# Performance work log

Measured on AMD Instinct MI355X. Metric: run time of the kernel, lower is better.

## Reference

```python
import jax, jax.numpy as jnp
import numpy as np

V = 50000   # nodes
E = 600000  # edges
D = 256     # node_feat_size == graph_feat_size
K = 20      # hardcoded Kronecker projection dim
OUT = 256   # out_dim

def layer_norm(x, g, b, eps=1e-5):
    mu = jnp.mean(x, axis=-1, keepdims=True)
    var = jnp.var(x, axis=-1, keepdims=True)
    return (x - mu) * jax.lax.rsqrt(var + eps) * g + b

def setup_inputs() -> dict:
    key = jax.random.key(0)
    ks = jax.random.split(key, 12)
    def rn(k, shape, s=0.05):
        return jax.random.normal(k, shape, dtype=jnp.float32) * s
    return dict(
        node_feats=jax.random.normal(ks[0], (V, D), dtype=jnp.float32),
        src=jax.random.randint(ks[1], (E,), 0, V),
        dst=jax.random.randint(ks[2], (E,), 0, V),
        # KroneckerMessage.proj_node: Linear(D,20)+LN(20)
        Wp=rn(ks[3], (D, K)), bp=jnp.zeros((K,), jnp.float32),
        gp=jnp.ones((K,), jnp.float32), betap=jnp.zeros((K,), jnp.float32),
        # KroneckerMessage.proj_kron: Linear(400,OUT)+LN(OUT)
        Wk=rn(ks[4], (K * K, OUT)), bk=jnp.zeros((OUT,), jnp.float32),
        gk=jnp.ones((OUT,), jnp.float32), betak=jnp.zeros((OUT,), jnp.float32),
        # project_edge: Linear(2D,1)
        We=rn(ks[5], (2 * D, 1)), be=jnp.zeros((1,), jnp.float32),
        # AttentiveGRU2.project_node: Linear(D, graph_feat_size=D)
        Wn=rn(ks[6], (D, D)), bn=jnp.zeros((D,), jnp.float32),
        # GRUCell(input=D, hidden=D), torch layout [3H, in]
        W_ih=rn(ks[7], (3 * D, D)), W_hh=rn(ks[8], (3 * D, D)),
        b_ih=jnp.zeros((3 * D,), jnp.float32), b_hh=jnp.zeros((3 * D,), jnp.float32),
        # layer_norm after GRU
        g_ln=jnp.ones((D,), jnp.float32), beta_ln=jnp.zeros((D,), jnp.float32),
        # concat_proj: Linear(D+OUT, D)+LN(D)
        Wc=rn(ks[9], (D + OUT, D)), bc=jnp.zeros((D,), jnp.float32),
        gc=jnp.ones((D,), jnp.float32), betac=jnp.zeros((D,), jnp.float32),
    )

def reference(node_feats, src, dst, Wp, bp, gp, betap, Wk, bk, gk, betak,
              We, be, Wn, bn, W_ih, W_hh, b_ih, b_hh, g_ln, beta_ln,
              Wc, bc, gc, betac):
    Vn = node_feats.shape[0]
    En = src.shape[0]
    # --- KroneckerMessage branch ---
    npj = jax.nn.relu(layer_norm(node_feats @ Wp + bp, gp, betap))        # [V, 20]
    kron = jnp.einsum('ea,ek->eak', npj[src], npj[dst]).reshape(En, -1)    # [E, 400]
    kron = jax.nn.relu(layer_norm(kron @ Wk + bk, gk, betak))              # [E, OUT]
    kron_feat = jax.ops.segment_sum(kron, dst, num_segments=Vn)           # [V, OUT]
    # --- edge attention logits (he = [dst_hv, src_hv]) ---
    he = jnp.concatenate([node_feats[dst], node_feats[src]], axis=1)       # [E, 2D]
    logits = jax.nn.relu(he @ We + be)                                     # [E, 1]
    # --- edge softmax grouped by destination node ---
    m = jax.ops.segment_max(logits, dst, num_segments=Vn)                  # [V, 1]
    ex = jnp.exp(logits - m[dst])
    denom = jax.ops.segment_sum(ex, dst, num_segments=Vn)
    a = ex / denom[dst]                                                    # [E, 1]
    # --- weighted src-feature aggregation ---
    hv = node_feats @ Wn + bn                                              # [V, D]
    context = jax.nn.relu(jax.ops.segment_sum(hv[src] * a, dst, num_segments=Vn))
    # --- GRUCell(context, node_feats), torch semantics ---
    gi = context @ W_ih.T + b_ih
    gh = node_feats @ W_hh.T + b_hh
    i_r, i_z, i_n = jnp.split(gi, 3, axis=1)
    h_r, h_z, h_n = jnp.split(gh, 3, axis=1)
    r = jax.nn.sigmoid(i_r + h_r)
    z = jax.nn.sigmoid(i_z + h_z)
    n = jnp.tanh(i_n + r * h_n)
    h = (1.0 - z) * n + z * node_feats
    gru_out = layer_norm(jax.nn.relu(h), g_ln, beta_ln)                    # [V, D]
    # --- concat + projection ---
    cat = jnp.concatenate([gru_out, kron_feat], axis=1)                    # [V, D+OUT]
    return jax.nn.relu(layer_norm(cat @ Wc + bc, gc, betac))               # [V, D]
```

## Files before the change

### kernel.cpp

```cpp
#include <hip/hip_runtime.h>
#include <hip/hip_bf16.h>
#include <math.h>

#define KG 8
#define KTHR 512
#define KCHUNK 128

typedef __attribute__((ext_vector_type(8))) short bfrag;
typedef __attribute__((ext_vector_type(4))) float cfrag;
typedef _Float16 __attribute__((ext_vector_type(2))) half2v;

__device__ __forceinline__ ushort f2bf(float f) {
    __hip_bfloat16 h = __float2bfloat16(f);
    return *(ushort*)&h;
}
__device__ __forceinline__ float bf2f(ushort u) {
    __hip_bfloat16 h;
    *(ushort*)&h = u;
    return __bfloat162float(h);
}
__device__ __forceinline__ uint packf16(float lo, float hi) {
    _Float16 l = (_Float16)lo, h = (_Float16)hi;
    ushort ul = *(ushort*)&l, uh = *(ushort*)&h;
    return (uint)ul | ((uint)uh << 16);
}

__device__ __forceinline__ void blockSum2(float& s1, float& s2, float* red) {
    #pragma unroll
    for (int off = 32; off > 0; off >>= 1) {
        s1 += __shfl_xor(s1, off);
        s2 += __shfl_xor(s2, off);
    }
    int lane = threadIdx.x & 63, wid = threadIdx.x >> 6;
    if (lane == 0) { red[wid] = s1; red[4 + wid] = s2; }
    __syncthreads();
    s1 = red[0] + red[1] + red[2] + red[3];
    s2 = red[4] + red[5] + red[6] + red[7];
}

__device__ __forceinline__ float dppWaveSum(float x) {
    float t;
    t = __int_as_float(__builtin_amdgcn_update_dpp(0, __float_as_int(x), 0x111, 0xf, 0xf, true)); x += t;
    t = __int_as_float(__builtin_amdgcn_update_dpp(0, __float_as_int(x), 0x112, 0xf, 0xf, true)); x += t;
    t = __int_as_float(__builtin_amdgcn_update_dpp(0, __float_as_int(x), 0x114, 0xf, 0xf, true)); x += t;
    t = __int_as_float(__builtin_amdgcn_update_dpp(0, __float_as_int(x), 0x118, 0xf, 0xf, true)); x += t;
    t = __int_as_float(__builtin_amdgcn_update_dpp(0, __float_as_int(x), 0x142, 0xf, 0xf, true)); x += t;
    t = __int_as_float(__builtin_amdgcn_update_dpp(0, __float_as_int(x), 0x143, 0xf, 0xf, true)); x += t;
    return __int_as_float(__builtin_amdgcn_readlane(__float_as_int(x), 63));
}

__device__ __forceinline__ float sigmoidf(float x) { return 1.0f / (1.0f + expf(-x)); }

__global__ __launch_bounds__(256) void cast_bf16_kernel(
    const float* __restrict__ x, ushort* __restrict__ y, int n)
{
    int i = (blockIdx.x * 256 + threadIdx.x) * 4;
    if (i < n) {
        float4 v = *(const float4*)(x + i);
        ushort4 o;
        o.x = f2bf(v.x); o.y = f2bf(v.y); o.z = f2bf(v.z); o.w = f2bf(v.w);
        *(ushort4*)(y + i) = o;
    }
}

__global__ __launch_bounds__(256) void prep_w_kernel(
    const float* __restrict__ Wn, const float* __restrict__ Wih,
    const float* __restrict__ Whh, const float* __restrict__ Wc,
    const float* __restrict__ b_ih, const float* __restrict__ b_hh,
    const float* __restrict__ Wp, const float* __restrict__ bp,
    const float* __restrict__ Wk,
    ushort* __restrict__ BTn, ushort* __restrict__ BTrz,
    ushort* __restrict__ BTin, ushort* __restrict__ BThn,
    ushort* __restrict__ BTc, float* __restrict__ bias_rz,
    ushort* __restrict__ BTp, float* __restrict__ bp_pad,
    uint* __restrict__ Wkp)
{
    int id = blockIdx.x * 256 + threadIdx.x;
    if (id < 262144) {
        int n = id >> 9, k = id & 511;
        float v = (k < 256) ? Wih[n * 256 + k] : Whh[n * 256 + k - 256];
        BTrz[id] = f2bf(v);
    } else if (id < 327680) {
        int j = id - 262144; int n = j >> 8, k = j & 255;
        BTin[j] = f2bf(Wih[(512 + n) * 256 + k]);
    } else if (id < 393216) {
        int j = id - 327680; int n = j >> 8, k = j & 255;
        BThn[j] = f2bf(Whh[(512 + n) * 256 + k]);
    } else if (id < 458752) {
        int j = id - 393216; int n = j >> 8, k = j & 255;
        BTn[j] = f2bf(Wn[k * 256 + n]);
    } else if (id < 589824) {
        int j = id - 458752; int n = j >> 9, k = j & 511;
        BTc[j] = f2bf(Wc[k * 256 + n]);
    } else if (id < 590336) {
        int n = id - 589824;
        bias_rz[n] = b_ih[n] + b_hh[n];
    } else if (id < 623104) {
        int j = id - 590336; int n = j >> 8, k = j & 255;
        BTp[j] = f2bf((n < 20) ? Wp[k * 20 + n] : 0.f);
    } else if (id < 623232) {
        int n = id - 623104;
        bp_pad[n] = (n < 20) ? bp[n] : 0.f;
    } else if (id < 674432) {
        int j = id - 623232;
        int row = j >> 8, o = j & 255;
        int a = row / 10, kk = row - a * 10;
        float lo = Wk[(size_t)(a * 20 + 2 * kk) * 256 + o];
        float hi = Wk[(size_t)(a * 20 + 2 * kk + 1) * 256 + o];
        Wkp[j] = packf16(lo, hi);
    }
}

__global__ __launch_bounds__(256) void mfma_gemm_kernel(
    const ushort* __restrict__ A1, const ushort* __restrict__ A2, int ksplit, int lda,
    const ushort* __restrict__ B, const float* __restrict__ bias,
    void* __restrict__ Cout, int store_bf16,
    int M, int N, int K, int ldc)
{
    __shared__ ushort As[128 * 64];
    __shared__ ushort Bs[128 * 64];
    int t = threadIdx.x;
    int m0 = blockIdx.x * 128, n0 = blockIdx.y * 128;
    int w = t >> 6, lane = t & 63;
    int q = lane >> 4, r = lane & 15;
    int wm = (w & 1) * 64, wn = (w >> 1) * 64;

    cfrag acc[4][4] = {};

    int srow_base = t >> 3;
    int skc = t & 7;

    for (int k0 = 0; k0 < K; k0 += 64) {
        const ushort* Ap; int kb;
        if (k0 < ksplit) { Ap = A1; kb = k0; } else { Ap = A2; kb = k0 - ksplit; }
        int4 av[4], bv[4];
        #pragma unroll
        for (int i = 0; i < 4; ++i) {
            int row = i * 32 + srow_base;
            int grow = m0 + row;
            av[i] = make_int4(0, 0, 0, 0);
            if (grow < M) av[i] = *(const int4*)(Ap + (size_t)grow * lda + kb + skc * 8);
            bv[i] = *(const int4*)(B + (size_t)(n0 + row) * K + k0 + skc * 8);
        }
        __syncthreads();
        #pragma unroll
        for (int i = 0; i < 4; ++i) {
            int row = i * 32 + srow_base;
            int off = row * 64 + ((skc ^ (row & 7)) * 8);
            *(int4*)&As[off] = av[i];
            *(int4*)&Bs[off] = bv[i];
        }
        __syncthreads();
        #pragma unroll
        for (int s = 0; s < 2; ++s) {
            bfrag af[4], bfr[4];
            int kc = s * 4 + q;
            #pragma unroll
            for (int mi = 0; mi < 4; ++mi) {
                int arow = wm + mi * 16 + r;
                af[mi] = *(const bfrag*)&As[arow * 64 + ((kc ^ (arow & 7)) * 8)];
            }
            #pragma unroll
            for (int ni = 0; ni < 4; ++ni) {
                int brow = wn + ni * 16 + r;
                bfr[ni] = *(const bfrag*)&Bs[brow * 64 + ((kc ^ (brow & 7)) * 8)];
            }
            #pragma unroll
            for (int mi = 0; mi < 4; ++mi)
                #pragma unroll
                for (int ni = 0; ni < 4; ++ni)
                    acc[mi][ni] = __builtin_amdgcn_mfma_f32_16x16x32_bf16(
                        af[mi], bfr[ni], acc[mi][ni], 0, 0, 0);
        }
    }

    float bvld[4];
    #pragma unroll
    for (int ni = 0; ni < 4; ++ni) bvld[ni] = bias[n0 + wn + ni * 16 + r];
    #pragma unroll
    for (int mi = 0; mi < 4; ++mi) {
        #pragma unroll
        for (int v = 0; v < 4; ++v) {
            int grow = m0 + wm + mi * 16 + q * 4 + v;
            if (grow >= M) continue;
            #pragma unroll
            for (int ni = 0; ni < 4; ++ni) {
                int gcol = n0 + wn + ni * 16 + r;
                if (gcol >= N) continue;
                float val = acc[mi][ni][v] + bvld[ni];
                if (store_bf16) ((ushort*)Cout)[(size_t)grow * ldc + gcol] = f2bf(val);
                else            ((float*)Cout)[(size_t)grow * ldc + gcol] = val;
            }
        }
    }
}

__global__ __launch_bounds__(256) void ln20_kernel(
    const float* __restrict__ npj32, const float* __restrict__ gp,
    const float* __restrict__ betap, float* __restrict__ npj, int V)
{
    int wid = threadIdx.x >> 6, j = threadIdx.x & 63;
    int v = blockIdx.x * 4 + wid;
    if (v >= V) return;
    float acc = (j < 20) ? npj32[(size_t)v * 32 + j] : 0.f;
    float s1 = acc, s2 = acc * acc;
    #pragma unroll
    for (int off = 32; off > 0; off >>= 1) {
        s1 += __shfl_xor(s1, off);
        s2 += __shfl_xor(s2, off);
    }
    float mu = s1 * (1.0f / 20.0f);
    float var = s2 * (1.0f / 20.0f) - mu * mu;
    if (j < 20) {
        float y = (acc - mu) * rsqrtf(var + 1e-5f) * gp[j] + betap[j];
        npj[(size_t)v * 20 + j] = fmaxf(y, 0.f);
    }
}

__global__ __launch_bounds__(256) void deg_kernel(const int* __restrict__ dst, int* __restrict__ deg, int E) {
    int e = blockIdx.x * 256 + threadIdx.x;
    if (e < E) atomicAdd(&deg[dst[e]], 1);
}

__global__ __launch_bounds__(1024) void scan_kernel(const int* __restrict__ deg, int* __restrict__ row, int V) {
    __shared__ int wsum[16];
    __shared__ int carry_sh;
    int t = threadIdx.x, lane = t & 63, wid = t >> 6;
    if (t == 0) carry_sh = 0;
    __syncthreads();
    for (int base = 0; base < V; base += 1024) {
        int i = base + t;
        int val = (i < V) ? deg[i] : 0;
        #pragma unroll
        for (int s = 1; s < 64; s <<= 1) {
            int n = __shfl_up(val, s);
            if (lane >= s) val += n;
        }
        if (lane == 63) wsum[wid] = val;
        __syncthreads();
        if (wid == 0) {
            int x = (lane < 16) ? wsum[lane] : 0;
            #pragma unroll
            for (int s = 1; s < 16; s <<= 1) {
                int n = __shfl_up(x, s);
                if (lane >= s) x += n;
            }
            if (lane < 16) wsum[lane] = x;
        }
        __syncthreads();
        int wprefix = (wid > 0) ? wsum[wid - 1] : 0;
        int c = carry_sh;
        int incl = c + wprefix + val;
        if (i < V) row[i + 1] = incl;
        __syncthreads();
        if (t == 1023) carry_sh = incl;
    }
    if (t == 0) row[0] = 0;
}

__global__ __launch_bounds__(256) void scatter_kernel(
    const int* __restrict__ dst, const int* __restrict__ row,
    int* __restrict__ cnt, int* __restrict__ eorder, int E)
{
    int e = blockIdx.x * 256 + threadIdx.x;
    if (e < E) {
        int d = dst[e];
        int pos = row[d] + atomicAdd(&cnt[d], 1);
        eorder[pos] = e;
    }
}

__global__ __launch_bounds__(256) void nodeproj_kernel(
    const float* __restrict__ nf, const float* __restrict__ We,
    float* __restrict__ pd, float* __restrict__ ps, int V)
{
    int wid = threadIdx.x >> 6, lane = threadIdx.x & 63;
    int v = blockIdx.x * 4 + wid;
    if (v >= V) return;
    const float* row = nf + (size_t)v * 256;
    int i = lane * 4;
    float4 x  = *(const float4*)(row + i);
    float4 wd = *(const float4*)(We + i);
    float4 wsv = *(const float4*)(We + 256 + i);
    float sd = x.x * wd.x + x.y * wd.y + x.z * wd.z + x.w * wd.w;
    float ss = x.x * wsv.x + x.y * wsv.y + x.z * wsv.z + x.w * wsv.w;
    #pragma unroll
    for (int off = 32; off > 0; off >>= 1) {
        sd += __shfl_xor(sd, off);
        ss += __shfl_xor(ss, off);
    }
    if (lane == 0) { pd[v] = sd; ps[v] = ss; }
}

__global__ __launch_bounds__(256) void edgeprep_kernel(
    const int* __restrict__ eorder, const int* __restrict__ src, const int* __restrict__ dst,
    const float* __restrict__ pd, const float* __restrict__ ps, const float* __restrict__ be,
    float* __restrict__ logitOrd, int* __restrict__ srcOrd, int E)
{
    int p = blockIdx.x * 256 + threadIdx.x;
    if (p < E) {
        int e = eorder[p];
        int s = src[e], d = dst[e];
        srcOrd[p] = s;
        logitOrd[p] = fmaxf(pd[d] + ps[s] + be[0], 0.f);
    }
}

__global__ __launch_bounds__(KTHR) void kron_kernel(
    const float* __restrict__ npj, const int* __restrict__ srcOrd,
    const int* __restrict__ rowPtr,
    const uint* __restrict__ Wkp, const float* __restrict__ bk,
    const float* __restrict__ gkv, const float* __restrict__ betak,
    ushort* __restrict__ acat, int V)
{
    __shared__ __hip_bfloat16 T[KG * 20 * 256];
    __shared__ uint dshp[KG * 10];
    __shared__ float sE[KCHUNK * 20];
    int t = threadIdx.x;
    int v0 = blockIdx.x * KG;

    if (t < KG * 10) {
        int g = t / 10, kk = t - g * 10;
        int v = v0 + g;
        float lo = 0.f, hi = 0.f;
        if (v < V) {
            lo = npj[(size_t)v * 20 + 2 * kk];
            hi = npj[(size_t)v * 20 + 2 * kk + 1];
        }
        dshp[t] = packf16(lo, hi);
    }
    __syncthreads();

    {
        uint dreg[KG][10];
        #pragma unroll
        for (int g = 0; g < KG; ++g)
            #pragma unroll
            for (int kk = 0; kk < 10; ++kk) dreg[g][kk] = dshp[g * 10 + kk];

        int c = t & 255, h = t >> 8;
        int a0 = h * 10;
        for (int a = a0; a < a0 + 10; ++a) {
            uint wv[10];
            #pragma unroll
            for (int kk = 0; kk < 10; ++kk)
                wv[kk] = Wkp[(size_t)(a * 10 + kk) * 256 + c];
            #pragma unroll
            for (int g = 0; g < KG; ++g) {
                float s = 0.f;
                #pragma unroll
                for (int kk = 0; kk < 10; ++kk) {
                    half2v d2 = *(half2v*)&dreg[g][kk];
                    half2v w2 = *(half2v*)&wv[kk];
                    s = __builtin_amdgcn_fdot2(d2, w2, s, false);
                }
                T[(g * 20 + a) * 256 + c] = __float2bfloat16(s);
            }
        }
    }
    __syncthreads();

    int wid = t >> 6, lane = t & 63;
    int v = v0 + wid;
    int c0 = lane * 4;

    float Tr[20][4];
    #pragma unroll
    for (int a = 0; a < 20; ++a) {
        const __hip_bfloat16* tp = &T[(wid * 20 + a) * 256 + c0];
        Tr[a][0] = __bfloat162float(tp[0]);
        Tr[a][1] = __bfloat162float(tp[1]);
        Tr[a][2] = __bfloat162float(tp[2]);
        Tr[a][3] = __bfloat162float(tp[3]);
    }
    float4 bkv = *(const float4*)(bk + c0);
    float4 gk4 = *(const float4*)(gkv + c0);
    float4 bt4 = *(const float4*)(betak + c0);

    int eBase = rowPtr[v0];
    int vEnd = (v0 + KG < V) ? (v0 + KG) : V;
    int eEndB = rowPtr[vEnd];
    int myE0 = (v < V) ? rowPtr[v] : 0;
    int myE1 = (v < V) ? rowPtr[v + 1] : 0;

    float a0 = 0.f, a1 = 0.f, a2 = 0.f, a3 = 0.f;

    for (int base = eBase; base < eEndB; base += KCHUNK) {
        int nC = eEndB - base; if (nC > KCHUNK) nC = KCHUNK;
        __syncthreads();
        for (int idx = t; idx < nC * 20; idx += KTHR) {
            int le = idx / 20, aa = idx - le * 20;
            sE[idx] = npj[(size_t)srcOrd[base + le] * 20 + aa];
        }
        __syncthreads();

        int lo = (myE0 > base) ? myE0 : base;
        int hi = (myE1 < base + nC) ? myE1 : base + nC;
        int p = lo;
        for (; p + 1 < hi; p += 2) {
            const float* sa = &sE[(p - base) * 20];
            const float* sb = &sE[(p + 1 - base) * 20];
            float4 sa0 = *(const float4*)(sa);
            float4 sa1 = *(const float4*)(sa + 4);
            float4 sa2 = *(const float4*)(sa + 8);
            float4 sa3 = *(const float4*)(sa + 12);
            float4 sa4 = *(const float4*)(sa + 16);
            float4 sb0 = *(const float4*)(sb);
            float4 sb1 = *(const float4*)(sb + 4);
            float4 sb2 = *(const float4*)(sb + 8);
            float4 sb3 = *(const float4*)(sb + 12);
            float4 sb4 = *(const float4*)(sb + 16);
            float sav[20] = {sa0.x, sa0.y, sa0.z, sa0.w, sa1.x, sa1.y, sa1.z, sa1.w,
                             sa2.x, sa2.y, sa2.z, sa2.w, sa3.x, sa3.y, sa3.z, sa3.w,
                             sa4.x, sa4.y, sa4.z, sa4.w};
            float sbv[20] = {sb0.x, sb0.y, sb0.z, sb0.w, sb1.x, sb1.y, sb1.z, sb1.w,
                             sb2.x, sb2.y, sb2.z, sb2.w, sb3.x, sb3.y, sb3.z, sb3.w,
                             sb4.x, sb4.y, sb4.z, sb4.w};
            float ya0 = bkv.x, ya1 = bkv.y, ya2 = bkv.z, ya3 = bkv.w;
            float yb0 = bkv.x, yb1 = bkv.y, yb2 = bkv.z, yb3 = bkv.w;
            #pragma unroll
            for (int a = 0; a < 20; ++a) {
                float va = sav[a], vb = sbv[a];
                ya0 += va * Tr[a][0]; ya1 += va * Tr[a][1];
                ya2 += va * Tr[a][2]; ya3 += va * Tr[a][3];
                yb0 += vb * Tr[a][0]; yb1 += vb * Tr[a][1];
                yb2 += vb * Tr[a][2]; yb3 += vb * Tr[a][3];
            }
            float s1a = dppWaveSum(ya0 + ya1 + ya2 + ya3);
            float s2a = dppWaveSum(ya0 * ya0 + ya1 * ya1 + ya2 * ya2 + ya3 * ya3);
            float s1b = dppWaveSum(yb0 + yb1 + yb2 + yb3);
            float s2b = dppWaveSum(yb0 * yb0 + yb1 * yb1 + yb2 * yb2 + yb3 * yb3);
            float mua = s1a * (1.0f / 256.0f);
            float rsa = rsqrtf(s2a * (1.0f / 256.0f) - mua * mua + 1e-5f);
            float mub = s1b * (1.0f / 256.0f);
            float rsb = rsqrtf(s2b * (1.0f / 256.0f) - mub * mub + 1e-5f);
            a0 += fmaxf((ya0 - mua) * rsa * gk4.x + bt4.x, 0.f) + fmaxf((yb0 - mub) * rsb * gk4.x + bt4.x, 0.f);
            a1 += fmaxf((ya1 - mua) * rsa * gk4.y + bt4.y, 0.f) + fmaxf((yb1 - mub) * rsb * gk4.y + bt4.y, 0.f);
            a2 += fmaxf((ya2 - mua) * rsa * gk4.z + bt4.z, 0.f) + fmaxf((yb2 - mub) * rsb * gk4.z + bt4.z, 0.f);
            a3 += fmaxf((ya3 - mua) * rsa * gk4.w + bt4.w, 0.f) + fmaxf((yb3 - mub) * rsb * gk4.w + bt4.w, 0.f);
        }
        if (p < hi) {
            const float* sa = &sE[(p - base) * 20];
            float4 sa0 = *(const float4*)(sa);
            float4 sa1 = *(const float4*)(sa + 4);
            float4 sa2 = *(const float4*)(sa + 8);
            float4 sa3 = *(const float4*)(sa + 12);
            float4 sa4 = *(const float4*)(sa + 16);
            float sav[20] = {sa0.x, sa0.y, sa0.z, sa0.w, sa1.x, sa1.y, sa1.z, sa1.w,
                             sa2.x, sa2.y, sa2.z, sa2.w, sa3.x, sa3.y, sa3.z, sa3.w,
                             sa4.x, sa4.y, sa4.z, sa4.w};
            float ya0 = bkv.x, ya1 = bkv.y, ya2 = bkv.z, ya3 = bkv.w;
            #pragma unroll
            for (int a = 0; a < 20; ++a) {
                float va = sav[a];
                ya0 += va * Tr[a][0]; ya1 += va * Tr[a][1];
                ya2 += va * Tr[a][2]; ya3 += va * Tr[a][3];
            }
            float s1a = dppWaveSum(ya0 + ya1 + ya2 + ya3);
            float s2a = dppWaveSum(ya0 * ya0 + ya1 * ya1 + ya2 * ya2 + ya3 * ya3);
            float mua = s1a * (1.0f / 256.0f);
            float rsa = rsqrtf(s2a * (1.0f / 256.0f) - mua * mua + 1e-5f);
            a0 += fmaxf((ya0 - mua) * rsa * gk4.x + bt4.x, 0.f);
            a1 += fmaxf((ya1 - mua) * rsa * gk4.y + bt4.y, 0.f);
            a2 += fmaxf((ya2 - mua) * rsa * gk4.z + bt4.z, 0.f);
            a3 += fmaxf((ya3 - mua) * rsa * gk4.w + bt4.w, 0.f);
        }
    }
    if (v < V) {
        ushort4 o;
        o.x = f2bf(a0); o.y = f2bf(a1); o.z = f2bf(a2); o.w = f2bf(a3);
        *(ushort4*)(acat + (size_t)v * 512 + 256 + c0) = o;
    }
}

__global__ __launch_bounds__(256) void att_kernel(
    const float* __restrict__ logitOrd, const int* __restrict__ rowPtr,
    float* __restrict__ mArr, float* __restrict__ invArr, int V)
{
    int wid = threadIdx.x >> 6, lane = threadIdx.x & 63;
    int v = blockIdx.x * 4 + wid;
    if (v >= V) return;
    int e0 = rowPtr[v], e1 = rowPtr[v + 1];
    float m = -1e30f;
    for (int p = e0 + lane; p < e1; p += 64) m = fmaxf(m, logitOrd[p]);
    #pragma unroll
    for (int off = 32; off > 0; off >>= 1) m = fmaxf(m, __shfl_xor(m, off));
    float d = 0.f;
    for (int p = e0 + lane; p < e1; p += 64) d += expf(logitOrd[p] - m);
    #pragma unroll
    for (int off = 32; off > 0; off >>= 1) d += __shfl_xor(d, off);
    if (lane == 0) {
        mArr[v] = m;
        invArr[v] = (e1 > e0) ? (1.0f / d) : 0.f;
    }
}

__global__ __launch_bounds__(256) void ctx_kernel(
    const ushort* __restrict__ hv_bf, const float* __restrict__ logitOrd,
    const float* __restrict__ mArr, const float* __restrict__ invArr,
    const int* __restrict__ srcOrd, const int* __restrict__ rowPtr,
    ushort* __restrict__ ctx_bf, int V)
{
    int v = blockIdx.x;
    int t = threadIdx.x;
    int e0 = rowPtr[v], e1 = rowPtr[v + 1];
    float m = mArr[v], inv = invArr[v];
    float acc = 0.f;
    int p = e0;
    for (; p + 3 < e1; p += 4) {
        int s0 = srcOrd[p], s1 = srcOrd[p + 1], s2 = srcOrd[p + 2], s3 = srcOrd[p + 3];
        float w0 = expf(logitOrd[p] - m) * inv;
        float w1 = expf(logitOrd[p + 1] - m) * inv;
        float w2 = expf(logitOrd[p + 2] - m) * inv;
        float w3 = expf(logitOrd[p + 3] - m) * inv;
        float h0 = bf2f(hv_bf[(size_t)s0 * 256 + t]);
        float h1 = bf2f(hv_bf[(size_t)s1 * 256 + t]);
        float h2 = bf2f(hv_bf[(size_t)s2 * 256 + t]);
        float h3 = bf2f(hv_bf[(size_t)s3 * 256 + t]);
        acc += w0 * h0 + w1 * h1 + w2 * h2 + w3 * h3;
    }
    for (; p < e1; ++p) {
        float wgt = expf(logitOrd[p] - m) * inv;
        acc += wgt * bf2f(hv_bf[(size_t)srcOrd[p] * 256 + t]);
    }
    ctx_bf[(size_t)v * 256 + t] = f2bf(fmaxf(acc, 0.f));
}

__global__ __launch_bounds__(256) void gru_ln_kernel(
    const ushort* __restrict__ rz, const ushort* __restrict__ inb,
    const ushort* __restrict__ hnb, const float* __restrict__ nf,
    const float* __restrict__ g_ln, const float* __restrict__ b_ln,
    ushort* __restrict__ acat, int V)
{
    __shared__ float red[8];
    int v = blockIdx.x, t = threadIdx.x;
    float r = sigmoidf(bf2f(rz[(size_t)v * 512 + t]));
    float z = sigmoidf(bf2f(rz[(size_t)v * 512 + 256 + t]));
    float n = tanhf(bf2f(inb[(size_t)v * 256 + t]) + r * bf2f(hnb[(size_t)v * 256 + t]));
    float h = (1.f - z) * n + z * nf[(size_t)v * 256 + t];
    float x = fmaxf(h, 0.f);
    float s1 = x, s2 = x * x;
    blockSum2(s1, s2, red);
    float mu = s1 * (1.0f / 256.0f);
    float var = s2 * (1.0f / 256.0f) - mu * mu;
    float y = (x - mu) * rsqrtf(var + 1e-5f) * g_ln[t] + b_ln[t];
    acat[(size_t)v * 512 + t] = f2bf(y);
}

__global__ __launch_bounds__(256) void ln_kernel(
    const float* __restrict__ in, float* __restrict__ out,
    const float* __restrict__ g, const float* __restrict__ b, int relu_after)
{
    __shared__ float red[8];
    int v = blockIdx.x, t = threadIdx.x;
    float x = in[(size_t)v * 256 + t];
    float s1 = x, s2 = x * x;
    blockSum2(s1, s2, red);
    float mu = s1 * (1.0f / 256.0f);
    float var = s2 * (1.0f / 256.0f) - mu * mu;
    float y = (x - mu) * rsqrtf(var + 1e-5f) * g[t] + b[t];
    if (relu_after) y = fmaxf(y, 0.f);
    out[(size_t)v * 256 + t] = y;
}

extern "C" void kernel_launch(void* const* d_in, const int* in_sizes, int n_in,
                              void* d_out, int out_size, void* d_ws, size_t ws_size,
                              hipStream_t stream)
{
    const float* nf    = (const float*)d_in[0];
    const int*   src   = (const int*)d_in[1];
    const int*   dst   = (const int*)d_in[2];
    const float* Wp    = (const float*)d_in[3];
    const float* bp    = (const float*)d_in[4];
    const float* gp    = (const float*)d_in[5];
    const float* betap = (const float*)d_in[6];
    const float* Wk    = (const float*)d_in[7];
    const float* bk    = (const float*)d_in[8];
    const float* gk    = (const float*)d_in[9];
    const float* betak = (const float*)d_in[10];
    const float* We    = (const float*)d_in[11];
    const float* be    = (const float*)d_in[12];
    const float* Wn    = (const float*)d_in[13];
    const float* bn    = (const float*)d_in[14];
    const float* W_ih  = (const float*)d_in[15];
    const float* W_hh  = (const float*)d_in[16];
    const float* b_ih  = (const float*)d_in[17];
    const float* b_hh  = (const float*)d_in[18];
    const float* g_ln  = (const float*)d_in[19];
    const float* bt_ln = (const float*)d_in[20];
    const float* Wc    = (const float*)d_in[21];
    const float* bc    = (const float*)d_in[22];
    const float* gc    = (const float*)d_in[23];
    const float* betac = (const float*)d_in[24];

    int V = in_sizes[0] / 256;
    int E = in_sizes[1];

    char* w = (char*)d_ws;
    auto alloc = [&](size_t bytes) -> char* {
        char* p = w;
        w += (bytes + 255) & ~(size_t)255;
        return p;
    };
    float*  npj      = (float*)alloc((size_t)V * 20 * 4);
    float*  npj32    = (float*)alloc((size_t)V * 32 * 4);
    ushort* acat     = (ushort*)alloc((size_t)V * 512 * 2);
    ushort* nf_bf    = (ushort*)alloc((size_t)V * 256 * 2);
    ushort* ctx_bf   = (ushort*)alloc((size_t)V * 256 * 2);
    ushort* rz_bf    = (ushort*)alloc((size_t)V * 512 * 2);
    ushort* hv_bf    = rz_bf;
    ushort* in_bf    = (ushort*)alloc((size_t)V * 256 * 2);
    ushort* hn_bf    = (ushort*)alloc((size_t)V * 256 * 2);
    ushort* BTn      = (ushort*)alloc(65536 * 2);
    ushort* BTrz     = (ushort*)alloc(262144 * 2);
    ushort* BTin     = (ushort*)alloc(65536 * 2);
    ushort* BThn     = (ushort*)alloc(65536 * 2);
    ushort* BTc      = (ushort*)alloc(131072 * 2);
    ushort* BTp      = (ushort*)alloc(32768 * 2);
    float*  bias_rz  = (float*)alloc(512 * 4);
    float*  bp_pad   = (float*)alloc(128 * 4);
    float*  logitOrd = (float*)alloc((size_t)E * 4);
    int*    srcOrd   = (int*)alloc((size_t)E * 4);
    float*  pd       = (float*)alloc((size_t)V * 4);
    float*  ps       = (float*)alloc((size_t)V * 4);
    float*  mArr     = (float*)alloc((size_t)V * 4);
    float*  invArr   = (float*)alloc((size_t)V * 4);
    int*    deg      = (int*)alloc((size_t)V * 4);
    int*    cnt      = (int*)alloc((size_t)V * 4);
    int*    rowp     = (int*)alloc((size_t)(V + 1) * 4);
    int*    eorder   = (int*)alloc((size_t)E * 4);
    uint*   Wkp      = (uint*)alloc((size_t)51200 * 4);

    hipMemsetAsync(deg, 0, (size_t)V * 4, stream);
    hipMemsetAsync(cnt, 0, (size_t)V * 4, stream);

    int mt = (V + 127) / 128;

    cast_bf16_kernel<<<(V * 64 + 255) / 256, 256, 0, stream>>>(nf, nf_bf, V * 256);
    prep_w_kernel<<<(674432 + 255) / 256, 256, 0, stream>>>(
        Wn, W_ih, W_hh, Wc, b_ih, b_hh, Wp, bp, Wk,
        BTn, BTrz, BTin, BThn, BTc, bias_rz, BTp, bp_pad, Wkp);

    mfma_gemm_kernel<<<dim3(mt, 1), 256, 0, stream>>>(
        nf_bf, nf_bf, 256, 256, BTp, bp_pad, npj32, 0, V, 32, 256, 32);
    ln20_kernel<<<(V + 3) / 4, 256, 0, stream>>>(npj32, gp, betap, npj, V);

    deg_kernel<<<(E + 255) / 256, 256, 0, stream>>>(dst, deg, E);
    scan_kernel<<<1, 1024, 0, stream>>>(deg, rowp, V);
    scatter_kernel<<<(E + 255) / 256, 256, 0, stream>>>(dst, rowp, cnt, eorder, E);
    nodeproj_kernel<<<(V + 3) / 4, 256, 0, stream>>>(nf, We, pd, ps, V);
    edgeprep_kernel<<<(E + 255) / 256, 256, 0, stream>>>(
        eorder, src, dst, pd, ps, be, logitOrd, srcOrd, E);

    mfma_gemm_kernel<<<dim3(mt, 2), 256, 0, stream>>>(
        nf_bf, nf_bf, 256, 256, BTn, bn, hv_bf, 1, V, 256, 256, 256);
    att_kernel<<<(V + 3) / 4, 256, 0, stream>>>(logitOrd, rowp, mArr, invArr, V);
    ctx_kernel<<<V, 256, 0, stream>>>(hv_bf, logitOrd, mArr, invArr, srcOrd, rowp, ctx_bf, V);

    kron_kernel<<<(V + KG - 1) / KG, KTHR, 0, stream>>>(
        npj, srcOrd, rowp, Wkp, bk, gk, betak, acat, V);

    mfma_gemm_kernel<<<dim3(mt, 4), 256, 0, stream>>>(
        ctx_bf, nf_bf, 256, 256, BTrz, bias_rz, rz_bf, 1, V, 512, 512, 512);
    mfma_gemm_kernel<<<dim3(mt, 2), 256, 0, stream>>>(
        ctx_bf, ctx_bf, 256, 256, BTin, b_ih + 512, in_bf, 1, V, 256, 256, 256);
    mfma_gemm_kernel<<<dim3(mt, 2), 256, 0, stream>>>(
        nf_bf, nf_bf, 256, 256, BThn, b_hh + 512, hn_bf, 1, V, 256, 256, 256);

    gru_ln_kernel<<<V, 256, 0, stream>>>(rz_bf, in_bf, hn_bf, nf, g_ln, bt_ln, acat, V);

    mfma_gemm_kernel<<<dim3(mt, 2), 256, 0, stream>>>(
        acat, acat, 512, 512, BTc, bc, (float*)d_out, 0, V, 256, 512, 256);
    ln_kernel<<<V, 256, 0, stream>>>((float*)d_out, (float*)d_out, gc, betac, 1);
}
```

Before: 1.227 ms.

## Use packed fp16 dot2 for per-edge Kronecker projection and process four edges per iteration

The per-destination T table is now stored as packed fp16 pairs, and gathered source projections are packed into fp16 pairs in shared memory. The per-edge 20-term dot product becomes 10 fdot2 instructions, which halves the FMA count and the LDS traffic. The edge loop is unrolled to four edges so their wave reductions can interleave. In exchange, T and the source features lose precision (fp16 instead of bf16/fp32 inputs) and register pressure rises.

After: 1.119 ms. 1.1x faster.

```diff
diff --git a/kernel.cpp b/kernel.cpp
--- a/kernel.cpp
+++ b/kernel.cpp
@@ -313,9 +313,9 @@
     const float* __restrict__ gkv, const float* __restrict__ betak,
     ushort* __restrict__ acat, int V)
 {
-    __shared__ __hip_bfloat16 T[KG * 20 * 256];
+    __shared__ uint T16[KG * 10 * 256];
     __shared__ uint dshp[KG * 10];
-    __shared__ float sE[KCHUNK * 20];
+    __shared__ uint sEp[KCHUNK * 12];
     int t = threadIdx.x;
     int v0 = blockIdx.x * KG;
 
@@ -339,22 +339,25 @@
             for (int kk = 0; kk < 10; ++kk) dreg[g][kk] = dshp[g * 10 + kk];
 
         int c = t & 255, h = t >> 8;
-        int a0 = h * 10;
-        for (int a = a0; a < a0 + 10; ++a) {
-            uint wv[10];
-            #pragma unroll
-            for (int kk = 0; kk < 10; ++kk)
-                wv[kk] = Wkp[(size_t)(a * 10 + kk) * 256 + c];
+        int kk0 = h * 5;
+        for (int kk = kk0; kk < kk0 + 5; ++kk) {
+            uint wv0[10], wv1[10];
+            #pragma unroll
+            for (int j = 0; j < 10; ++j)
+                wv0[j] = Wkp[(size_t)((2 * kk) * 10 + j) * 256 + c];
+            #pragma unroll
+            for (int j = 0; j < 10; ++j)
+                wv1[j] = Wkp[(size_t)((2 * kk + 1) * 10 + j) * 256 + c];
             #pragma unroll
             for (int g = 0; g < KG; ++g) {
-                float s = 0.f;
+                float s0 = 0.f, s1 = 0.f;
                 #pragma unroll
-                for (int kk = 0; kk < 10; ++kk) {
-                    half2v d2 = *(half2v*)&dreg[g][kk];
-                    half2v w2 = *(half2v*)&wv[kk];
-                    s = __builtin_amdgcn_fdot2(d2, w2, s, false);
+                for (int j = 0; j < 10; ++j) {
+                    half2v d2 = *(half2v*)&dreg[g][j];
+                    s0 = __builtin_amdgcn_fdot2(d2, *(half2v*)&wv0[j], s0, false);
+                    s1 = __builtin_amdgcn_fdot2(d2, *(half2v*)&wv1[j], s1, false);
                 }
-                T[(g * 20 + a) * 256 + c] = __float2bfloat16(s);
+                T16[(g * 10 + kk) * 256 + c] = packf16(s0, s1);
             }
         }
     }
@@ -364,14 +367,19 @@
     int v = v0 + wid;
     int c0 = lane * 4;
 
-    float Tr[20][4];
-    #pragma unroll
-    for (int a = 0; a < 20; ++a) {
-        const __hip_bfloat16* tp = &T[(wid * 20 + a) * 256 + c0];
-        Tr[a][0] = __bfloat162float(tp[0]);
-        Tr[a][1] = __bfloat162float(tp[1]);
-        Tr[a][2] = __bfloat162float(tp[2]);
-        Tr[a][3] = __bfloat162float(tp[3]);
+    uint Tp[10][4];
+    if (v < V) {
+        #pragma unroll
+        for (int kk = 0; kk < 10; ++kk) {
+            int4 tv = *(const int4*)&T16[(wid * 10 + kk) * 256 + c0];
+            Tp[kk][0] = (uint)tv.x; Tp[kk][1] = (uint)tv.y;
+            Tp[kk][2] = (uint)tv.z; Tp[kk][3] = (uint)tv.w;
+        }
+    } else {
+        #pragma unroll
+        for (int kk = 0; kk < 10; ++kk) {
+            Tp[kk][0] = 0u; Tp[kk][1] = 0u; Tp[kk][2] = 0u; Tp[kk][3] = 0u;
+        }
     }
     float4 bkv = *(const float4*)(bk + c0);
     float4 gk4 = *(const float4*)(gkv + c0);
@@ -388,82 +396,85 @@
     for (int base = eBase; base < eEndB; base += KCHUNK) {
         int nC = eEndB - base; if (nC > KCHUNK) nC = KCHUNK;
         __syncthreads();
-        for (int idx = t; idx < nC * 20; idx += KTHR) {
-            int le = idx / 20, aa = idx - le * 20;
-            sE[idx] = npj[(size_t)srcOrd[base + le] * 20 + aa];
+        for (int idx = t; idx < nC * 10; idx += KTHR) {
+            int le = idx / 10, kk = idx - le * 10;
+            float2 v2 = *(const float2*)(npj + (size_t)srcOrd[base + le] * 20 + 2 * kk);
+            sEp[le * 12 + kk] = packf16(v2.x, v2.y);
         }
         __syncthreads();
 
         int lo = (myE0 > base) ? myE0 : base;
         int hi = (myE1 < base + nC) ? myE1 : base + nC;
         int p = lo;
-        for (; p + 1 < hi; p += 2) {
-            const float* sa = &sE[(p - base) * 20];
-            const float* sb = &sE[(p + 1 - base) * 20];
-            float4 sa0 = *(const float4*)(sa);
-            float4 sa1 = *(const float4*)(sa + 4);
-            float4 sa2 = *(const float4*)(sa + 8);
-            float4 sa3 = *(const float4*)(sa + 12);
-            float4 sa4 = *(const float4*)(sa + 16);
-            float4 sb0 = *(const float4*)(sb);
-            float4 sb1 = *(const float4*)(sb + 4);
-            float4 sb2 = *(const float4*)(sb + 8);
-            float4 sb3 = *(const float4*)(sb + 12);
-            float4 sb4 = *(const float4*)(sb + 16);
-            float sav[20] = {sa0.x, sa0.y, sa0.z, sa0.w, sa1.x, sa1.y, sa1.z, sa1.w,
-                             sa2.x, sa2.y, sa2.z, sa2.w, sa3.x, sa3.y, sa3.z, sa3.w,
-                             sa4.x, sa4.y, sa4.z, sa4.w};
-            float sbv[20] = {sb0.x, sb0.y, sb0.z, sb0.w, sb1.x, sb1.y, sb1.z, sb1.w,
-                             sb2.x, sb2.y, sb2.z, sb2.w, sb3.x, sb3.y, sb3.z, sb3.w,
-                             sb4.x, sb4.y, sb4.z, sb4.w};
-            float ya0 = bkv.x, ya1 = bkv.y, ya2 = bkv.z, ya3 = bkv.w;
-            float yb0 = bkv.x, yb1 = bkv.y, yb2 = bkv.z, yb3 = bkv.w;
-            #pragma unroll
-            for (int a = 0; a < 20; ++a) {
-                float va = sav[a], vb = sbv[a];
-                ya0 += va * Tr[a][0]; ya1 += va * Tr[a][1];
-                ya2 += va * Tr[a][2]; ya3 += va * Tr[a][3];
-                yb0 += vb * Tr[a][0]; yb1 += vb * Tr[a][1];
-                yb2 += vb * Tr[a][2]; yb3 += vb * Tr[a][3];
-            }
-            float s1a = dppWaveSum(ya0 + ya1 + ya2 + ya3);
-            float s2a = dppWaveSum(ya0 * ya0 + ya1 * ya1 + ya2 * ya2 + ya3 * ya3);
-            float s1b = dppWaveSum(yb0 + yb1 + yb2 + yb3);
-            float s2b = dppWaveSum(yb0 * yb0 + yb1 * yb1 + yb2 * yb2 + yb3 * yb3);
-            float mua = s1a * (1.0f / 256.0f);
-            float rsa = rsqrtf(s2a * (1.0f / 256.0f) - mua * mua + 1e-5f);
-            float mub = s1b * (1.0f / 256.0f);
-            float rsb = rsqrtf(s2b * (1.0f / 256.0f) - mub * mub + 1e-5f);
-            a0 += fmaxf((ya0 - mua) * rsa * gk4.x + bt4.x, 0.f) + fmaxf((yb0 - mub) * rsb * gk4.x + bt4.x, 0.f);
-            a1 += fmaxf((ya1 - mua) * rsa * gk4.y + bt4.y, 0.f) + fmaxf((yb1 - mub) * rsb * gk4.y + bt4.y, 0.f);
-            a2 += fmaxf((ya2 - mua) * rsa * gk4.z + bt4.z, 0.f) + fmaxf((yb2 - mub) * rsb * gk4.z + bt4.z, 0.f);
-            a3 += fmaxf((ya3 - mua) * rsa * gk4.w + bt4.w, 0.f) + fmaxf((yb3 - mub) * rsb * gk4.w + bt4.w, 0.f);
-        }
-        if (p < hi) {
-            const float* sa = &sE[(p - base) * 20];
-            float4 sa0 = *(const float4*)(sa);
-            float4 sa1 = *(const float4*)(sa + 4);
-            float4 sa2 = *(const float4*)(sa + 8);
-            float4 sa3 = *(const float4*)(sa + 12);
-            float4 sa4 = *(const float4*)(sa + 16);
-            float sav[20] = {sa0.x, sa0.y, sa0.z, sa0.w, sa1.x, sa1.y, sa1.z, sa1.w,
-                             sa2.x, sa2.y, sa2.z, sa2.w, sa3.x, sa3.y, sa3.z, sa3.w,
-                             sa4.x, sa4.y, sa4.z, sa4.w};
-            float ya0 = bkv.x, ya1 = bkv.y, ya2 = bkv.z, ya3 = bkv.w;
-            #pragma unroll
-            for (int a = 0; a < 20; ++a) {
-                float va = sav[a];
-                ya0 += va * Tr[a][0]; ya1 += va * Tr[a][1];
-                ya2 += va * Tr[a][2]; ya3 += va * Tr[a][3];
-            }
-            float s1a = dppWaveSum(ya0 + ya1 + ya2 + ya3);
-            float s2a = dppWaveSum(ya0 * ya0 + ya1 * ya1 + ya2 * ya2 + ya3 * ya3);
-            float mua = s1a * (1.0f / 256.0f);
-            float rsa = rsqrtf(s2a * (1.0f / 256.0f) - mua * mua + 1e-5f);
-            a0 += fmaxf((ya0 - mua) * rsa * gk4.x + bt4.x, 0.f);
-            a1 += fmaxf((ya1 - mua) * rsa * gk4.y + bt4.y, 0.f);
-            a2 += fmaxf((ya2 - mua) * rsa * gk4.z + bt4.z, 0.f);
-            a3 += fmaxf((ya3 - mua) * rsa * gk4.w + bt4.w, 0.f);
+        for (; p + 3 < hi; p += 4) {
+            float ya[4][4];
+            #pragma unroll
+            for (int e = 0; e < 4; ++e) {
+                const uint* sp = &sEp[(p + e - base) * 12];
+                int4 w0 = *(const int4*)(sp);
+                int4 w1 = *(const int4*)(sp + 4);
+                int2 w2 = *(const int2*)(sp + 8);
+                uint sv[10] = {(uint)w0.x, (uint)w0.y, (uint)w0.z, (uint)w0.w,
+                               (uint)w1.x, (uint)w1.y, (uint)w1.z, (uint)w1.w,
+                               (uint)w2.x, (uint)w2.y};
+                ya[e][0] = bkv.x; ya[e][1] = bkv.y; ya[e][2] = bkv.z; ya[e][3] = bkv.w;
+                #pragma unroll
+                for (int kk = 0; kk < 10; ++kk) {
+                    half2v s2h = *(half2v*)&sv[kk];
+                    ya[e][0] = __builtin_amdgcn_fdot2(s2h, *(half2v*)&Tp[kk][0], ya[e][0], false);
+                    ya[e][1] = __builtin_amdgcn_fdot2(s2h, *(half2v*)&Tp[kk][1], ya[e][1], false);
+                    ya[e][2] = __builtin_amdgcn_fdot2(s2h, *(half2v*)&Tp[kk][2], ya[e][2], false);
+                    ya[e][3] = __builtin_amdgcn_fdot2(s2h, *(half2v*)&Tp[kk][3], ya[e][3], false);
+                }
+            }
+            float pre1[4], pre2[4];
+            #pragma unroll
+            for (int e = 0; e < 4; ++e) {
+                pre1[e] = ya[e][0] + ya[e][1] + ya[e][2] + ya[e][3];
+                pre2[e] = ya[e][0] * ya[e][0] + ya[e][1] * ya[e][1]
+                        + ya[e][2] * ya[e][2] + ya[e][3] * ya[e][3];
+            }
+            float s1v[4], s2v[4];
+            #pragma unroll
+            for (int e = 0; e < 4; ++e) {
+                s1v[e] = dppWaveSum(pre1[e]);
+                s2v[e] = dppWaveSum(pre2[e]);
+            }
+            #pragma unroll
+            for (int e = 0; e < 4; ++e) {
+                float mu = s1v[e] * (1.0f / 256.0f);
+                float rs = rsqrtf(s2v[e] * (1.0f / 256.0f) - mu * mu + 1e-5f);
+                a0 += fmaxf((ya[e][0] - mu) * rs * gk4.x + bt4.x, 0.f);
+                a1 += fmaxf((ya[e][1] - mu) * rs * gk4.y + bt4.y, 0.f);
+                a2 += fmaxf((ya[e][2] - mu) * rs * gk4.z + bt4.z, 0.f);
+                a3 += fmaxf((ya[e][3] - mu) * rs * gk4.w + bt4.w, 0.f);
+            }
+        }
+        for (; p < hi; ++p) {
+            const uint* sp = &sEp[(p - base) * 12];
+            int4 w0 = *(const int4*)(sp);
+            int4 w1 = *(const int4*)(sp + 4);
+            int2 w2 = *(const int2*)(sp + 8);
+            uint sv[10] = {(uint)w0.x, (uint)w0.y, (uint)w0.z, (uint)w0.w,
+                           (uint)w1.x, (uint)w1.y, (uint)w1.z, (uint)w1.w,
+                           (uint)w2.x, (uint)w2.y};
+            float y0 = bkv.x, y1 = bkv.y, y2 = bkv.z, y3 = bkv.w;
+            #pragma unroll
+            for (int kk = 0; kk < 10; ++kk) {
+                half2v s2h = *(half2v*)&sv[kk];
+                y0 = __builtin_amdgcn_fdot2(s2h, *(half2v*)&Tp[kk][0], y0, false);
+                y1 = __builtin_amdgcn_fdot2(s2h, *(half2v*)&Tp[kk][1], y1, false);
+                y2 = __builtin_amdgcn_fdot2(s2h, *(half2v*)&Tp[kk][2], y2, false);
+                y3 = __builtin_amdgcn_fdot2(s2h, *(half2v*)&Tp[kk][3], y3, false);
+            }
+            float s1 = dppWaveSum(y0 + y1 + y2 + y3);
+            float s2 = dppWaveSum(y0 * y0 + y1 * y1 + y2 * y2 + y3 * y3);
+            float mu = s1 * (1.0f / 256.0f);
+            float rs = rsqrtf(s2 * (1.0f / 256.0f) - mu * mu + 1e-5f);
+            a0 += fmaxf((y0 - mu) * rs * gk4.x + bt4.x, 0.f);
+            a1 += fmaxf((y1 - mu) * rs * gk4.y + bt4.y, 0.f);
+            a2 += fmaxf((y2 - mu) * rs * gk4.z + bt4.z, 0.f);
+            a3 += fmaxf((y3 - mu) * rs * gk4.w + bt4.w, 0.f);
         }
     }
     if (v < V) {
```
